# Performance work log

Measured on AMD Instinct MI355X. Metric: run time of the kernel, lower is better.

The kernel has to match this reference:

```python
import jax, jax.numpy as jnp
import numpy as np

B = 4          # per_gpu_batch_size
P = 16         # n_contexts
N = B * P      # fused passage dim = 64
L = 512        # seq_len
H = 768        # hidden_size
S = 16         # sentence spans per passage


def setup_inputs() -> dict:
    key = jax.random.key(0)
    k1, k2, k3 = jax.random.split(key, 3)
    hidden_states = jax.random.normal(k1, (N, L, H), jnp.float32)
    # nn.Linear weight [out, in]; original init std=1.0 saturates tanh, use 0.02 scale for sane numerics
    dense_w = jax.random.normal(k2, (H, H), jnp.float32) * 0.02
    dense_b = jnp.zeros((H,), jnp.float32)
    attention_mask = jnp.ones((N, L), jnp.int32)
    # strictly increasing boundaries -> S non-empty, ragged, contiguous spans per passage
    r = jnp.sort(jax.random.randint(k3, (N, S + 1), 0, L - S), axis=-1) + jnp.arange(S + 1, dtype=jnp.int32)
    spans = jnp.stack([r[:, :-1], r[:, 1:]], axis=-1).astype(jnp.int32)  # [N, S, 2]
    return dict(hidden_states=hidden_states, dense_w=dense_w, dense_b=dense_b,
                attention_mask=attention_mask, spans=spans)


def reference(hidden_states, dense_w, dense_b, attention_mask, spans):
    # sentence_spans branch: token_tensor = hidden_states (all tokens)
    # pooled_output = activation(dense(token_tensor)); cls_norm_type == 'none' -> no norm
    pooled = jnp.tanh(jnp.einsum('nlh,oh->nlo', hidden_states, dense_w) + dense_b)  # [N, L, H]
    pooled_output_passages = pooled[:, 0]  # [N, H]
    # ragged per-span mean pooling, vectorized as a masked segment reduce
    pos = jnp.arange(L, dtype=jnp.int32)                         # [L]
    start = spans[..., 0][..., None]                             # [N, S, 1]
    end = spans[..., 1][..., None]                               # [N, S, 1]
    m = ((pos >= start) & (pos < end)).astype(pooled.dtype)      # [N, S, L]
    sums = jnp.einsum('nsl,nlh->nsh', m, pooled)                 # [N, S, H]
    counts = (spans[..., 1] - spans[..., 0]).astype(pooled.dtype)[..., None]  # [N, S, 1]
    sentence_embeddings = (sums / counts).reshape(N * S, H)      # [N*S, H]
    # all S spans valid per passage -> mask of zeros (0 = valid in original code)
    sentence_mask = jnp.zeros((N, S), jnp.float32)
    return pooled_output_passages, sentence_embeddings, sentence_mask
```

## Files before the change

kernel.cpp:

```cpp
#include <hip/hip_runtime.h>
#include <hip/hip_bf16.h>

#define NPASS 64
#define LSEQ  512
#define HDIM  768
#define NSPAN 16
#define MTOT  (NPASS*LSEQ)
#define OFF_SENT (NPASS*HDIM)
#define A_ELEMS (MTOT*HDIM)
#define W_ELEMS (HDIM*HDIM)

#define BM 128
#define BN 128
#define BK 32
#define NK (HDIM/BK)

typedef __bf16 bf16x8 __attribute__((ext_vector_type(8)));
typedef float  f32x4  __attribute__((ext_vector_type(4)));

__device__ inline unsigned short f2bf(float f) {
  __hip_bfloat16 h = __float2bfloat16(f);
  unsigned short u; __builtin_memcpy(&u, &h, 2); return u;
}

__device__ inline float fast_tanh(float x) {
  const float ax = fabsf(x);
  const float t  = __expf(-2.0f * ax);
  const float r  = (1.0f - t) * __builtin_amdgcn_rcpf(1.0f + t);
  return copysignf(r, x);
}

__global__ __launch_bounds__(256) void convert_kernel(
    const float* __restrict__ A, const float* __restrict__ W,
    unsigned short* __restrict__ Ab, unsigned short* __restrict__ Wb)
{
  const long long i = ((long long)blockIdx.x * 256 + threadIdx.x) * 8;
  const float* src; unsigned short* dst; long long off;
  if (i < A_ELEMS) { src = A; dst = Ab; off = i; }
  else             { src = W; dst = Wb; off = i - A_ELEMS; }
  const float4 a = *(const float4*)(src + off);
  const float4 b = *(const float4*)(src + off + 4);
  union { unsigned short us[8]; uint4 v; } o;
  o.us[0]=f2bf(a.x); o.us[1]=f2bf(a.y); o.us[2]=f2bf(a.z); o.us[3]=f2bf(a.w);
  o.us[4]=f2bf(b.x); o.us[5]=f2bf(b.y); o.us[6]=f2bf(b.z); o.us[7]=f2bf(b.w);
  *(uint4*)(dst + off) = o.v;
}

__global__ __launch_bounds__(256) void gemm_fused_kernel(
    const unsigned short* __restrict__ Ab,
    const unsigned short* __restrict__ Wb,
    const float* __restrict__ bias,
    const int* __restrict__ spans,
    float* __restrict__ out)
{
  __shared__ __align__(16) unsigned short As[2][BM*BK];
  __shared__ __align__(16) unsigned short Bs[2][BN*BK];
  __shared__ int   sp_st[NSPAN], sp_en[NSPAN];
  __shared__ float inv_s[NSPAN];
  __shared__ short sid_l[BM];
  __shared__ float bias_s[BN];

  const int tid  = threadIdx.x;
  const int wave = tid >> 6;
  const int lane = tid & 63;
  const int quad = lane >> 4;
  const int lr   = lane & 15;
  const int wm   = wave >> 1;
  const int wn   = wave & 1;
  const int tile_m = blockIdx.x * BM;
  const int tile_n = blockIdx.y * BN;
  const int npass  = tile_m >> 9;
  const int l0     = tile_m & 511;

  const int lrow = lane >> 2;
  const int lcol = (lane & 3) * 8;

  auto stage = [&](int k, int buf) {
    const int k0 = k * BK;
    #pragma unroll
    for (int j = 0; j < 4; ++j) {
      const int seg = wave * 4 + j;
      if (seg < 8) {
        const unsigned short* g =
            Ab + (size_t)(tile_m + seg * 16 + lrow) * HDIM + (k0 + lcol);
        __builtin_amdgcn_global_load_lds(
            (const __attribute__((address_space(1))) void*)g,
            (__attribute__((address_space(3))) void*)(As[buf] + seg * 512),
            16, 0, 0);
      } else {
        const int s2 = seg - 8;
        const unsigned short* g =
            Wb + (size_t)(tile_n + s2 * 16 + lrow) * HDIM + (k0 + lcol);
        __builtin_amdgcn_global_load_lds(
            (const __attribute__((address_space(1))) void*)g,
            (__attribute__((address_space(3))) void*)(Bs[buf] + s2 * 512),
            16, 0, 0);
      }
    }
  };

  stage(0, 0);
  if (tid < NSPAN) {
    const int st = spans[(npass * NSPAN + tid) * 2 + 0];
    const int en = spans[(npass * NSPAN + tid) * 2 + 1];
    sp_st[tid] = st; sp_en[tid] = en; inv_s[tid] = 1.0f / (float)(en - st);
  }
  if (tid >= 128 && tid < 128 + BN) bias_s[tid - 128] = bias[tile_n + tid - 128];
  __syncthreads();
  if (tid < BM) {
    const int l = l0 + tid;
    short s = -1;
    #pragma unroll
    for (int i = 0; i < NSPAN; ++i)
      if (l >= sp_st[i] && l < sp_en[i]) s = (short)i;
    sid_l[tid] = s;
  }

  f32x4 acc[4][4];
  #pragma unroll
  for (int i = 0; i < 4; ++i)
    #pragma unroll
    for (int j = 0; j < 4; ++j)
      acc[i][j] = (f32x4){0.f, 0.f, 0.f, 0.f};

  for (int k = 0; k < NK; ++k) {
    const int cur = k & 1;
    if (k + 1 < NK) stage(k + 1, cur ^ 1);

    bf16x8 af[4], bf[4];
    #pragma unroll
    for (int mt = 0; mt < 4; ++mt)
      af[mt] = *(const bf16x8*)(As[cur] + ((wm * 64 + mt * 16 + lr) * BK + quad * 8));
    #pragma unroll
    for (int nt = 0; nt < 4; ++nt)
      bf[nt] = *(const bf16x8*)(Bs[cur] + ((wn * 64 + nt * 16 + lr) * BK + quad * 8));

    #pragma unroll
    for (int mt = 0; mt < 4; ++mt)
      #pragma unroll
      for (int nt = 0; nt < 4; ++nt)
        acc[mt][nt] = __builtin_amdgcn_mfma_f32_16x16x32_bf16(
            af[mt], bf[nt], acc[mt][nt], 0, 0, 0);

    __syncthreads();
  }

  #pragma unroll
  for (int nt = 0; nt < 4; ++nt) {
    const int lcolo = wn * 64 + nt * 16 + lr;
    const int col   = tile_n + lcolo;
    const float bv  = bias_s[lcolo];
    float* sent_col = out + OFF_SENT + (size_t)(npass * NSPAN) * HDIM + col;
    #pragma unroll
    for (int mt = 0; mt < 4; ++mt) {
      const int rowbase = wm * 64 + mt * 16 + quad * 4;
      int prev = -1; float run = 0.f;
      #pragma unroll
      for (int r = 0; r < 4; ++r) {
        const int lrw = rowbase + r;
        const float v = fast_tanh(acc[mt][nt][r] + bv);
        if (l0 == 0 && lrw == 0) out[(size_t)npass * HDIM + col] = v;
        const int s = sid_l[lrw];
        if (s != prev) {
          if (prev >= 0) unsafeAtomicAdd(sent_col + (size_t)prev * HDIM, run * inv_s[prev]);
          prev = s; run = 0.f;
        }
        run += v;
      }
      if (prev >= 0) unsafeAtomicAdd(sent_col + (size_t)prev * HDIM, run * inv_s[prev]);
    }
  }
}

extern "C" void kernel_launch(void* const* d_in, const int* in_sizes, int n_in,
                              void* d_out, int out_size, void* d_ws, size_t ws_size,
                              hipStream_t stream) {
  const float* hs  = (const float*)d_in[0];
  const float* w   = (const float*)d_in[1];
  const float* bsc = (const float*)d_in[2];
  const int* spans = (const int*)d_in[4];
  float* out = (float*)d_out;

  unsigned short* Ab = (unsigned short*)d_ws;
  unsigned short* Wb = Ab + A_ELEMS;

  hipMemsetAsync(d_out, 0, (size_t)out_size * sizeof(float), stream);

  convert_kernel<<<dim3((A_ELEMS + W_ELEMS) / 8 / 256), dim3(256), 0, stream>>>(
      hs, w, Ab, Wb);

  dim3 grid(MTOT / BM, HDIM / BN);
  gemm_fused_kernel<<<grid, dim3(256), 0, stream>>>(Ab, Wb, bsc, spans, out);
}
```

Baseline: 267.4 us.

## Tile GEMM per whole passage and reduce spans in shared memory without atomics

The GEMM now uses 512x64 tiles so each block covers one full passage (all 512 tokens) and a 64-column strip, with 512 threads and a swizzled block order. The epilogue writes tanh outputs for each 16-column slice into LDS and then reduces every span directly, writing sentence means with plain stores instead of global atomics. This removes atomic contention and the need for partial sums across blocks. The cost is that each block must load a much larger A tile per k-step, uses about 72KB of LDS, and adds extra barriers in the epilogue.

Result: slower. 543.2 us (+103.1%).

```diff
diff --git a/kernel.cpp b/kernel.cpp
--- a/kernel.cpp
+++ b/kernel.cpp
@@ -10,10 +10,11 @@
 #define A_ELEMS (MTOT*HDIM)
 #define W_ELEMS (HDIM*HDIM)
 
-#define BM 128
-#define BN 128
+#define BM 512
+#define BN 64
 #define BK 32
 #define NK (HDIM/BK)
+#define NBLK (HDIM/BN)
 
 typedef __bf16 bf16x8 __attribute__((ext_vector_type(8)));
 typedef float  f32x4  __attribute__((ext_vector_type(4)));
@@ -46,18 +47,16 @@
   *(uint4*)(dst + off) = o.v;
 }
 
-__global__ __launch_bounds__(256) void gemm_fused_kernel(
+__global__ __launch_bounds__(512, 4) void gemm_fused_kernel(
     const unsigned short* __restrict__ Ab,
     const unsigned short* __restrict__ Wb,
     const float* __restrict__ bias,
     const int* __restrict__ spans,
     float* __restrict__ out)
 {
-  __shared__ __align__(16) unsigned short As[2][BM*BK];
-  __shared__ __align__(16) unsigned short Bs[2][BN*BK];
+  __shared__ __align__(16) unsigned char smem[73728];
   __shared__ int   sp_st[NSPAN], sp_en[NSPAN];
   __shared__ float inv_s[NSPAN];
-  __shared__ short sid_l[BM];
   __shared__ float bias_s[BN];
 
   const int tid  = threadIdx.x;
@@ -65,37 +64,38 @@
   const int lane = tid & 63;
   const int quad = lane >> 4;
   const int lr   = lane & 15;
-  const int wm   = wave >> 1;
-  const int wn   = wave & 1;
-  const int tile_m = blockIdx.x * BM;
-  const int tile_n = blockIdx.y * BN;
-  const int npass  = tile_m >> 9;
-  const int l0     = tile_m & 511;
+
+  const int b     = blockIdx.x;
+  const int rest  = b >> 3;
+  const int npass = (rest / NBLK) * 8 + (b & 7);
+  const int nb    = rest % NBLK;
+  const int tile_n = nb * BN;
+  const size_t arow0 = (size_t)npass * LSEQ;
 
   const int lrow = lane >> 2;
   const int lcol = (lane & 3) * 8;
 
   auto stage = [&](int k, int buf) {
     const int k0 = k * BK;
+    unsigned short* As = (unsigned short*)(smem + buf * 32768);
+    unsigned short* Bs = (unsigned short*)(smem + 65536 + buf * 4096);
     #pragma unroll
     for (int j = 0; j < 4; ++j) {
-      const int seg = wave * 4 + j;
-      if (seg < 8) {
-        const unsigned short* g =
-            Ab + (size_t)(tile_m + seg * 16 + lrow) * HDIM + (k0 + lcol);
-        __builtin_amdgcn_global_load_lds(
-            (const __attribute__((address_space(1))) void*)g,
-            (__attribute__((address_space(3))) void*)(As[buf] + seg * 512),
-            16, 0, 0);
-      } else {
-        const int s2 = seg - 8;
-        const unsigned short* g =
-            Wb + (size_t)(tile_n + s2 * 16 + lrow) * HDIM + (k0 + lcol);
-        __builtin_amdgcn_global_load_lds(
-            (const __attribute__((address_space(1))) void*)g,
-            (__attribute__((address_space(3))) void*)(Bs[buf] + s2 * 512),
-            16, 0, 0);
-      }
+      const int seg = wave + j * 8;
+      const unsigned short* g =
+          Ab + (arow0 + seg * 16 + lrow) * HDIM + (k0 + lcol);
+      __builtin_amdgcn_global_load_lds(
+          (const __attribute__((address_space(1))) void*)g,
+          (__attribute__((address_space(3))) void*)(As + seg * 512),
+          16, 0, 0);
+    }
+    if (wave < 4) {
+      const unsigned short* g =
+          Wb + (size_t)(tile_n + wave * 16 + lrow) * HDIM + (k0 + lcol);
+      __builtin_amdgcn_global_load_lds(
+          (const __attribute__((address_space(1))) void*)g,
+          (__attribute__((address_space(3))) void*)(Bs + wave * 512),
+          16, 0, 0);
     }
   };
 
@@ -107,14 +107,6 @@
   }
   if (tid >= 128 && tid < 128 + BN) bias_s[tid - 128] = bias[tile_n + tid - 128];
   __syncthreads();
-  if (tid < BM) {
-    const int l = l0 + tid;
-    short s = -1;
-    #pragma unroll
-    for (int i = 0; i < NSPAN; ++i)
-      if (l >= sp_st[i] && l < sp_en[i]) s = (short)i;
-    sid_l[tid] = s;
-  }
 
   f32x4 acc[4][4];
   #pragma unroll
@@ -127,13 +119,16 @@
     const int cur = k & 1;
     if (k + 1 < NK) stage(k + 1, cur ^ 1);
 
+    const unsigned short* As = (const unsigned short*)(smem + cur * 32768);
+    const unsigned short* Bs = (const unsigned short*)(smem + 65536 + cur * 4096);
+
     bf16x8 af[4], bf[4];
     #pragma unroll
     for (int mt = 0; mt < 4; ++mt)
-      af[mt] = *(const bf16x8*)(As[cur] + ((wm * 64 + mt * 16 + lr) * BK + quad * 8));
+      af[mt] = *(const bf16x8*)(As + ((wave * 64 + mt * 16 + lr) * BK + quad * 8));
     #pragma unroll
     for (int nt = 0; nt < 4; ++nt)
-      bf[nt] = *(const bf16x8*)(Bs[cur] + ((wn * 64 + nt * 16 + lr) * BK + quad * 8));
+      bf[nt] = *(const bf16x8*)(Bs + ((nt * 16 + lr) * BK + quad * 8));
 
     #pragma unroll
     for (int mt = 0; mt < 4; ++mt)
@@ -145,30 +140,29 @@
     __syncthreads();
   }
 
-  #pragma unroll
+  float* strip = (float*)smem;
+  #pragma unroll 1
   for (int nt = 0; nt < 4; ++nt) {
-    const int lcolo = wn * 64 + nt * 16 + lr;
-    const int col   = tile_n + lcolo;
-    const float bv  = bias_s[lcolo];
-    float* sent_col = out + OFF_SENT + (size_t)(npass * NSPAN) * HDIM + col;
+    const float bv = bias_s[nt * 16 + lr];
     #pragma unroll
-    for (int mt = 0; mt < 4; ++mt) {
-      const int rowbase = wm * 64 + mt * 16 + quad * 4;
-      int prev = -1; float run = 0.f;
+    for (int mt = 0; mt < 4; ++mt)
       #pragma unroll
       for (int r = 0; r < 4; ++r) {
-        const int lrw = rowbase + r;
-        const float v = fast_tanh(acc[mt][nt][r] + bv);
-        if (l0 == 0 && lrw == 0) out[(size_t)npass * HDIM + col] = v;
-        const int s = sid_l[lrw];
-        if (s != prev) {
-          if (prev >= 0) unsafeAtomicAdd(sent_col + (size_t)prev * HDIM, run * inv_s[prev]);
-          prev = s; run = 0.f;
-        }
-        run += v;
+        const int row = wave * 64 + mt * 16 + quad * 4 + r;
+        strip[row * 16 + lr] = fast_tanh(acc[mt][nt][r] + bv);
       }
-      if (prev >= 0) unsafeAtomicAdd(sent_col + (size_t)prev * HDIM, run * inv_s[prev]);
+    __syncthreads();
+    if (tid < 256) {
+      const int s = tid >> 4, c = tid & 15;
+      float sum = 0.f;
+      for (int l = sp_st[s]; l < sp_en[s]; ++l) sum += strip[l * 16 + c];
+      out[OFF_SENT + (size_t)(npass * NSPAN + s) * HDIM + tile_n + nt * 16 + c]
+          = sum * inv_s[s];
+    } else if (tid < 272) {
+      const int c = tid - 256;
+      out[(size_t)npass * HDIM + tile_n + nt * 16 + c] = strip[c];
     }
+    __syncthreads();
   }
 }
 
@@ -184,11 +178,11 @@
   unsigned short* Ab = (unsigned short*)d_ws;
   unsigned short* Wb = Ab + A_ELEMS;
 
-  hipMemsetAsync(d_out, 0, (size_t)out_size * sizeof(float), stream);
+  (void)hipMemsetAsync(d_out, 0, (size_t)out_size * sizeof(float), stream);
 
   convert_kernel<<<dim3((A_ELEMS + W_ELEMS) / 8 / 256), dim3(256), 0, stream>>>(
       hs, w, Ab, Wb);
 
-  dim3 grid(MTOT / BM, HDIM / BN);
-  gemm_fused_kernel<<<grid, dim3(256), 0, stream>>>(Ab, Wb, bsc, spans, out);
+  gemm_fused_kernel<<<dim3(NPASS * NBLK), dim3(512), 0, stream>>>(
+      Ab, Wb, bsc, spans, out);
 }
```

## Enlarge GEMM tiles to 256x256 with 512 threads and grouped block swizzle

Applied to the files above, without the earlier changes.

Doubles the block tile to 256x256, using eight waves per block with each wave computing a 128x64 sub-tile, and lays out shared memory manually in one 64KB buffer. It also launches a 1D grid with a grouped mapping, where eight consecutive blocks share the same N tile across different M rows, to improve L2 reuse. The aim is to raise arithmetic intensity and cut global and LDS traffic per FLOP. The cost is more registers (accumulators double to 128 floats), one block per CU, and fewer blocks: 128x3 = 384 versus 256 CUs, which leaves a wave-quantization tail.

Measured after the change: 272.5 us. No clear change (+1.9%).

```diff
diff --git a/kernel.cpp b/kernel.cpp
--- a/kernel.cpp
+++ b/kernel.cpp
@@ -10,10 +10,12 @@
 #define A_ELEMS (MTOT*HDIM)
 #define W_ELEMS (HDIM*HDIM)
 
-#define BM 128
-#define BN 128
+#define BM 256
+#define BN 256
 #define BK 32
 #define NK (HDIM/BK)
+#define MT_M (MTOT/BM)
+#define MT_N (HDIM/BN)
 
 typedef __bf16 bf16x8 __attribute__((ext_vector_type(8)));
 typedef float  f32x4  __attribute__((ext_vector_type(4)));
@@ -46,15 +48,14 @@
   *(uint4*)(dst + off) = o.v;
 }
 
-__global__ __launch_bounds__(256) void gemm_fused_kernel(
+__global__ __launch_bounds__(512, 1) void gemm_fused_kernel(
     const unsigned short* __restrict__ Ab,
     const unsigned short* __restrict__ Wb,
     const float* __restrict__ bias,
     const int* __restrict__ spans,
     float* __restrict__ out)
 {
-  __shared__ __align__(16) unsigned short As[2][BM*BK];
-  __shared__ __align__(16) unsigned short Bs[2][BN*BK];
+  __shared__ __align__(16) unsigned char smem[65536];
   __shared__ int   sp_st[NSPAN], sp_en[NSPAN];
   __shared__ float inv_s[NSPAN];
   __shared__ short sid_l[BM];
@@ -65,35 +66,43 @@
   const int lane = tid & 63;
   const int quad = lane >> 4;
   const int lr   = lane & 15;
-  const int wm   = wave >> 1;
-  const int wn   = wave & 1;
-  const int tile_m = blockIdx.x * BM;
-  const int tile_n = blockIdx.y * BN;
+  const int wm   = wave >> 2;
+  const int wn   = wave & 3;
+
+  const int b    = blockIdx.x;
+  const int rest = b >> 3;
+  const int mrow = (rest / MT_N) * 8 + (b & 7);
+  const int nb   = rest % MT_N;
+  const int tile_m = mrow * BM;
+  const int tile_n = nb * BN;
   const int npass  = tile_m >> 9;
   const int l0     = tile_m & 511;
+  const size_t arow0 = (size_t)tile_m;
 
   const int lrow = lane >> 2;
   const int lcol = (lane & 3) * 8;
 
   auto stage = [&](int k, int buf) {
     const int k0 = k * BK;
+    unsigned short* As = (unsigned short*)(smem + buf * 16384);
+    unsigned short* Bs = (unsigned short*)(smem + 32768 + buf * 16384);
     #pragma unroll
     for (int j = 0; j < 4; ++j) {
-      const int seg = wave * 4 + j;
-      if (seg < 8) {
+      const int seg = wave + j * 8;
+      if (seg < 16) {
         const unsigned short* g =
-            Ab + (size_t)(tile_m + seg * 16 + lrow) * HDIM + (k0 + lcol);
+            Ab + (arow0 + seg * 16 + lrow) * HDIM + (k0 + lcol);
         __builtin_amdgcn_global_load_lds(
             (const __attribute__((address_space(1))) void*)g,
-            (__attribute__((address_space(3))) void*)(As[buf] + seg * 512),
+            (__attribute__((address_space(3))) void*)(As + seg * 512),
             16, 0, 0);
       } else {
-        const int s2 = seg - 8;
+        const int s2 = seg - 16;
         const unsigned short* g =
             Wb + (size_t)(tile_n + s2 * 16 + lrow) * HDIM + (k0 + lcol);
         __builtin_amdgcn_global_load_lds(
             (const __attribute__((address_space(1))) void*)g,
-            (__attribute__((address_space(3))) void*)(Bs[buf] + s2 * 512),
+            (__attribute__((address_space(3))) void*)(Bs + s2 * 512),
             16, 0, 0);
       }
     }
@@ -105,7 +114,7 @@
     const int en = spans[(npass * NSPAN + tid) * 2 + 1];
     sp_st[tid] = st; sp_en[tid] = en; inv_s[tid] = 1.0f / (float)(en - st);
   }
-  if (tid >= 128 && tid < 128 + BN) bias_s[tid - 128] = bias[tile_n + tid - 128];
+  if (tid >= 256) bias_s[tid - 256] = bias[tile_n + tid - 256];
   __syncthreads();
   if (tid < BM) {
     const int l = l0 + tid;
@@ -116,9 +125,9 @@
     sid_l[tid] = s;
   }
 
-  f32x4 acc[4][4];
+  f32x4 acc[8][4];
   #pragma unroll
-  for (int i = 0; i < 4; ++i)
+  for (int i = 0; i < 8; ++i)
     #pragma unroll
     for (int j = 0; j < 4; ++j)
       acc[i][j] = (f32x4){0.f, 0.f, 0.f, 0.f};
@@ -127,16 +136,19 @@
     const int cur = k & 1;
     if (k + 1 < NK) stage(k + 1, cur ^ 1);
 
-    bf16x8 af[4], bf[4];
-    #pragma unroll
-    for (int mt = 0; mt < 4; ++mt)
-      af[mt] = *(const bf16x8*)(As[cur] + ((wm * 64 + mt * 16 + lr) * BK + quad * 8));
+    const unsigned short* As = (const unsigned short*)(smem + cur * 16384);
+    const unsigned short* Bs = (const unsigned short*)(smem + 32768 + cur * 16384);
+
+    bf16x8 af[8], bf[4];
+    #pragma unroll
+    for (int mt = 0; mt < 8; ++mt)
+      af[mt] = *(const bf16x8*)(As + ((wm * 128 + mt * 16 + lr) * BK + quad * 8));
     #pragma unroll
     for (int nt = 0; nt < 4; ++nt)
-      bf[nt] = *(const bf16x8*)(Bs[cur] + ((wn * 64 + nt * 16 + lr) * BK + quad * 8));
-
-    #pragma unroll
-    for (int mt = 0; mt < 4; ++mt)
+      bf[nt] = *(const bf16x8*)(Bs + ((wn * 64 + nt * 16 + lr) * BK + quad * 8));
+
+    #pragma unroll
+    for (int mt = 0; mt < 8; ++mt)
       #pragma unroll
       for (int nt = 0; nt < 4; ++nt)
         acc[mt][nt] = __builtin_amdgcn_mfma_f32_16x16x32_bf16(
@@ -152,8 +164,8 @@
     const float bv  = bias_s[lcolo];
     float* sent_col = out + OFF_SENT + (size_t)(npass * NSPAN) * HDIM + col;
     #pragma unroll
-    for (int mt = 0; mt < 4; ++mt) {
-      const int rowbase = wm * 64 + mt * 16 + quad * 4;
+    for (int mt = 0; mt < 8; ++mt) {
+      const int rowbase = wm * 128 + mt * 16 + quad * 4;
       int prev = -1; float run = 0.f;
       #pragma unroll
       for (int r = 0; r < 4; ++r) {
@@ -184,11 +196,11 @@
   unsigned short* Ab = (unsigned short*)d_ws;
   unsigned short* Wb = Ab + A_ELEMS;
 
-  hipMemsetAsync(d_out, 0, (size_t)out_size * sizeof(float), stream);
+  (void)hipMemsetAsync(d_out, 0, (size_t)out_size * sizeof(float), stream);
 
   convert_kernel<<<dim3((A_ELEMS + W_ELEMS) / 8 / 256), dim3(256), 0, stream>>>(
       hs, w, Ab, Wb);
 
-  dim3 grid(MTOT / BM, HDIM / BN);
-  gemm_fused_kernel<<<grid, dim3(256), 0, stream>>>(Ab, Wb, bsc, spans, out);
-}
+  gemm_fused_kernel<<<dim3(MT_M * MT_N), dim3(512), 0, stream>>>(
+      Ab, Wb, bsc, spans, out);
+}
```
